# Performance work log

Measured on AMD Instinct MI355X. Metric: run time of the kernel, lower is better.

The kernel has to match this reference:

```python
import jax, jax.numpy as jnp
import numpy as np

N, C, H, W = 4, 256, 64, 64
C_EMBED = C // 2  # 128

def setup_inputs() -> dict:
    key = jax.random.key(0)
    k1, k2, k3, k4 = jax.random.split(key, 4)
    x = jax.random.normal(k1, (N, C, H, W), dtype=jnp.float32)
    # 1x1 conv weights stored as [out_ch, in_ch] (torch Conv2d weight squeezed)
    theta_w = jax.random.normal(k2, (C_EMBED, C), dtype=jnp.float32) * 0.01
    phi_w = jax.random.normal(k3, (C_EMBED, C), dtype=jnp.float32) * 0.01
    proj_w = jax.random.normal(k4, (C, C), dtype=jnp.float32) * 0.01
    return {"x": x, "theta_w": theta_w, "phi_w": phi_w, "proj_w": proj_w}

def reference(x, theta_w, phi_w, proj_w):
    n, c, h, w = x.shape
    s = h * w
    xf = x.reshape(n, c, s)  # [n, c, s]
    theta = jnp.einsum('ec,ncs->nse', theta_w, xf)  # [n, s, e]
    phi = jnp.einsum('ec,ncs->nes', phi_w, xf)      # [n, e, s]
    scale = jnp.sqrt(jnp.float32(theta_w.shape[0]))
    f = jnp.einsum('nse,net->nst', theta, phi) / scale  # [n, s, s]
    f = jax.nn.softmax(f, axis=-1)
    y = jnp.einsum('nst,nct->ncs', f, xf)  # attend over g = x, -> [n, c, s]
    res = jnp.einsum('oc,ncs->nos', proj_w, y)  # 1x1 projection conv
    return x + res.reshape(n, c, h, w)
```

## Files before the change

kernel.cpp:

```cpp
#include <hip/hip_runtime.h>
#include <cstdint>
#include <cstddef>

#define NB 4
#define CH 256
#define SS 4096
#define EE 128
#define QSCALE 0.08838834764831845f

typedef __attribute__((ext_vector_type(8))) short bfrag;
typedef __attribute__((ext_vector_type(8))) unsigned short u16x8;
typedef __attribute__((ext_vector_type(8))) _Float16 h16x8;
typedef __attribute__((ext_vector_type(4))) float f32x4;

__device__ __forceinline__ unsigned short f2bf(float f) {
  union { float f; unsigned int u; } v; v.f = f;
  unsigned int u = v.u;
  unsigned int r = u + 0x7FFFu + ((u >> 16) & 1u);
  return (unsigned short)(r >> 16);
}

__device__ __forceinline__ void lds_barrier() {
  asm volatile("s_waitcnt lgkmcnt(0)" ::: "memory");
  __builtin_amdgcn_s_barrier();
}

__global__ __launch_bounds__(256) void cvt_w(
    const float* __restrict__ thw, const float* __restrict__ phw,
    const float* __restrict__ pw,
    unsigned short* __restrict__ thwb, unsigned short* __restrict__ phwb,
    unsigned short* __restrict__ pwb)
{
  const int nw4 = EE * CH / 4;
  const int np4 = CH * CH / 4;
  int i = blockIdx.x * 256 + threadIdx.x;
  const float* src; unsigned short* dst; int off;
  if      (i < nw4)           { src = thw; dst = thwb; off = i; }
  else if (i < 2 * nw4)       { src = phw; dst = phwb; off = i - nw4; }
  else if (i < 2 * nw4 + np4) { src = pw;  dst = pwb;  off = i - 2 * nw4; }
  else return;
  float4 v = reinterpret_cast<const float4*>(src)[off];
  ushort4 o;
  o.x = f2bf(v.x); o.y = f2bf(v.y); o.z = f2bf(v.z); o.w = f2bf(v.w);
  reinterpret_cast<ushort4*>(dst)[off] = o;
}

__global__ __launch_bounds__(512) void pass1_qk(
    const float* __restrict__ x,
    const unsigned short* __restrict__ thw,
    const unsigned short* __restrict__ phw,
    unsigned short* __restrict__ xb,
    unsigned short* __restrict__ Qt,
    unsigned short* __restrict__ Kt)
{
  __shared__ unsigned short xT[64][CH + 8];
  const int t  = threadIdx.x;
  const int n  = blockIdx.y;
  const int s0 = blockIdx.x * 64;

  {
    const int soff = (t & 15) * 4;
    const int c0   = t >> 4;
    #pragma unroll
    for (int ci = 0; ci < 8; ++ci) {
      const int c = c0 + ci * 32;
      const size_t rowoff = ((size_t)n * CH + c) * SS + s0;
      float4 v = reinterpret_cast<const float4*>(x + rowoff)[soff >> 2];
      ushort4 o;
      o.x = f2bf(v.x); o.y = f2bf(v.y); o.z = f2bf(v.z); o.w = f2bf(v.w);
      reinterpret_cast<ushort4*>(xb + rowoff)[soff >> 2] = o;
      xT[soff + 0][c] = o.x;
      xT[soff + 1][c] = o.y;
      xT[soff + 2][c] = o.z;
      xT[soff + 3][c] = o.w;
    }
  }
  __syncthreads();

  const int w    = t >> 6;
  const int lane = t & 63;
  const int q    = lane >> 4;
  const int mr   = lane & 15;
  const int wrow = (w & 3) * 16;
  const int half = w >> 2;

  bfrag a[8];
  {
    const bfrag* rp = reinterpret_cast<const bfrag*>(&xT[wrow + mr][0]);
    #pragma unroll
    for (int k = 0; k < 8; ++k) a[k] = rp[k * 4 + q];
  }

  const unsigned short* wsel = half ? phw : thw;
  unsigned short*       osel = half ? Kt  : Qt;
  const float           sc   = half ? 1.0f : QSCALE;
  const bfrag* wp = reinterpret_cast<const bfrag*>(wsel);
  #pragma unroll
  for (int nt = 0; nt < 8; ++nt) {
    f32x4 acc = {0.f, 0.f, 0.f, 0.f};
    #pragma unroll
    for (int k = 0; k < 8; ++k) {
      bfrag b = wp[(nt * 16 + mr) * (CH / 8) + k * 4 + q];
      acc = __builtin_amdgcn_mfma_f32_16x16x32_bf16(a[k], b, acc, 0, 0, 0);
    }
    #pragma unroll
    for (int i = 0; i < 4; ++i) {
      const int srow = s0 + wrow + q * 4 + i;
      osel[((size_t)n * SS + srow) * EE + nt * 16 + mr] = f2bf(acc[i] * sc);
    }
  }
}

__global__ __launch_bounds__(512, 2) void pass2a(
    const unsigned short* __restrict__ Qt,
    const unsigned short* __restrict__ Kt,
    const unsigned short* __restrict__ xb,
    void* __restrict__ Opart_,
    float* __restrict__ ML,
    int use32)
{
  __shared__ __align__(16) unsigned char SMEM[138752];
  float          (*S_lds)[132] = reinterpret_cast<float(*)[132]>(SMEM);
  unsigned short (*P_lds)[136] = reinterpret_cast<unsigned short(*)[136]>(SMEM + 67584);
  unsigned short (*Q_lds)[136] = reinterpret_cast<unsigned short(*)[136]>(SMEM + 102400);
  float* row_m     = reinterpret_cast<float*>(SMEM + 137216);
  float* row_l     = reinterpret_cast<float*>(SMEM + 137728);
  float* row_alpha = reinterpret_cast<float*>(SMEM + 138240);

  float*    Of32 = reinterpret_cast<float*>(Opart_);
  _Float16* Oh16 = reinterpret_cast<_Float16*>(Opart_);

  const int t     = threadIdx.x;
  const int id    = blockIdx.x;
  const int xcd   = id & 7;
  const int n     = xcd >> 1;
  const int h     = xcd & 1;
  const int qt    = id >> 3;
  const int s0    = qt * 128;
  const int kbase = h * 2048;

  const int w    = t >> 6;
  const int lane = t & 63;
  const int q    = lane >> 4;
  const int mr   = lane & 15;

  if (t < 128) { row_m[t] = -INFINITY; row_l[t] = 0.f; }

  {
    const int col = (t & 15) * 8;
    #pragma unroll
    for (int j = 0; j < 4; ++j) {
      const int row = (t >> 4) + j * 32;
      *reinterpret_cast<u16x8*>(&Q_lds[row][col]) =
          *reinterpret_cast<const u16x8*>(
              Qt + ((size_t)n * SS + s0 + row) * EE + col);
    }
  }

  f32x4 o_accA[4][2], o_accB[4][2];
  #pragma unroll
  for (int ms = 0; ms < 4; ++ms)
    #pragma unroll
    for (int nt = 0; nt < 2; ++nt) {
      o_accA[ms][nt] = (f32x4){0.f, 0.f, 0.f, 0.f};
      o_accB[ms][nt] = (f32x4){0.f, 0.f, 0.f, 0.f};
    }

  __syncthreads();

  bfrag kb[4];
  {
    const bfrag* rp = reinterpret_cast<const bfrag*>(
        Kt + ((size_t)n * SS + kbase + w * 16 + mr) * EE);
    #pragma unroll
    for (int k = 0; k < 4; ++k) kb[k] = rp[k * 4 + q];
  }

#define QK_HALF(RB)                                                          \
  do {                                                                       \
    _Pragma("unroll")                                                        \
    for (int ms = 0; ms < 4; ++ms) {                                         \
      f32x4 acc = {0.f, 0.f, 0.f, 0.f};                                      \
      _Pragma("unroll")                                                      \
      for (int k = 0; k < 4; ++k) {                                          \
        bfrag aq = *reinterpret_cast<const bfrag*>(                          \
            &Q_lds[(RB) + ms * 16 + mr][(k * 4 + q) * 8]);                   \
        acc = __builtin_amdgcn_mfma_f32_16x16x32_bf16(aq, kb[k], acc, 0,0,0);\
      }                                                                      \
      _Pragma("unroll")                                                      \
      for (int i = 0; i < 4; ++i)                                            \
        S_lds[(RB) + ms * 16 + q * 4 + i][w * 16 + mr] = acc[i];             \
    }                                                                        \
  } while (0)

#define PV_HALF(OACC, RB)                                                    \
  do {                                                                       \
    _Pragma("unroll")                                                        \
    for (int ms = 0; ms < 4; ++ms) {                                         \
      float al[4];                                                           \
      _Pragma("unroll")                                                      \
      for (int i = 0; i < 4; ++i) al[i] = row_alpha[(RB) + ms*16 + q*4 + i]; \
      _Pragma("unroll")                                                      \
      for (int nt = 0; nt < 2; ++nt)                                         \
        _Pragma("unroll")                                                    \
        for (int i = 0; i < 4; ++i) OACC[ms][nt][i] *= al[i];                \
    }                                                                        \
    _Pragma("unroll")                                                        \
    for (int kk = 0; kk < 4; ++kk) {                                         \
      bfrag pa[4];                                                           \
      _Pragma("unroll")                                                      \
      for (int ms = 0; ms < 4; ++ms)                                         \
        pa[ms] = reinterpret_cast<const bfrag*>(                             \
            &P_lds[(RB) + ms * 16 + mr][0])[kk * 4 + q];                     \
      _Pragma("unroll")                                                      \
      for (int nt = 0; nt < 2; ++nt)                                         \
        _Pragma("unroll")                                                    \
        for (int ms = 0; ms < 4; ++ms)                                       \
          OACC[ms][nt] = __builtin_amdgcn_mfma_f32_16x16x32_bf16(            \
              pa[ms], vb[kk][nt], OACC[ms][nt], 0, 0, 0);                    \
    }                                                                        \
  } while (0)

  for (int t0 = 0; t0 < 2048; t0 += 128) {
    bfrag vb[4][2];
    #pragma unroll
    for (int nt = 0; nt < 2; ++nt) {
      const int c = w * 32 + nt * 16 + mr;
      const bfrag* vp = reinterpret_cast<const bfrag*>(
          xb + ((size_t)n * CH + c) * SS + kbase + t0);
      #pragma unroll
      for (int kk = 0; kk < 4; ++kk) vb[kk][nt] = vp[kk * 4 + q];
    }

    QK_HALF(0);
    QK_HALF(64);
    lds_barrier();

    if (t0 + 128 < 2048) {
      const bfrag* rp = reinterpret_cast<const bfrag*>(
          Kt + ((size_t)n * SS + kbase + t0 + 128 + w * 16 + mr) * EE);
      #pragma unroll
      for (int k = 0; k < 4; ++k) kb[k] = rp[k * 4 + q];
    }

    #pragma unroll
    for (int sh = 0; sh < 2; ++sh) {
      const int r  = sh * 64 + (t >> 3);
      const int cg = t & 7;
      const float4* srow = reinterpret_cast<const float4*>(&S_lds[r][cg * 16]);
      float4 v0 = srow[0], v1 = srow[1], v2 = srow[2], v3 = srow[3];
      float vmax = fmaxf(fmaxf(fmaxf(v0.x, v0.y), fmaxf(v0.z, v0.w)),
                         fmaxf(fmaxf(v1.x, v1.y), fmaxf(v1.z, v1.w)));
      vmax = fmaxf(vmax, fmaxf(fmaxf(fmaxf(v2.x, v2.y), fmaxf(v2.z, v2.w)),
                               fmaxf(fmaxf(v3.x, v3.y), fmaxf(v3.z, v3.w))));
      vmax = fmaxf(vmax, __shfl_xor(vmax, 1, 8));
      vmax = fmaxf(vmax, __shfl_xor(vmax, 2, 8));
      vmax = fmaxf(vmax, __shfl_xor(vmax, 4, 8));
      const float m_old = row_m[r];
      const float m_new = fmaxf(m_old, vmax);

      float p[16];
      p[0]=__expf(v0.x-m_new); p[1]=__expf(v0.y-m_new); p[2]=__expf(v0.z-m_new); p[3]=__expf(v0.w-m_new);
      p[4]=__expf(v1.x-m_new); p[5]=__expf(v1.y-m_new); p[6]=__expf(v1.z-m_new); p[7]=__expf(v1.w-m_new);
      p[8]=__expf(v2.x-m_new); p[9]=__expf(v2.y-m_new); p[10]=__expf(v2.z-m_new); p[11]=__expf(v2.w-m_new);
      p[12]=__expf(v3.x-m_new); p[13]=__expf(v3.y-m_new); p[14]=__expf(v3.z-m_new); p[15]=__expf(v3.w-m_new);
      float sum = 0.f;
      u16x8 pk0, pk1;
      #pragma unroll
      for (int j = 0; j < 8; ++j) { sum += p[j];     pk0[j] = f2bf(p[j]); }
      #pragma unroll
      for (int j = 0; j < 8; ++j) { sum += p[8 + j]; pk1[j] = f2bf(p[8 + j]); }
      *reinterpret_cast<u16x8*>(&P_lds[r][cg * 16])     = pk0;
      *reinterpret_cast<u16x8*>(&P_lds[r][cg * 16 + 8]) = pk1;
      sum += __shfl_xor(sum, 1, 8);
      sum += __shfl_xor(sum, 2, 8);
      sum += __shfl_xor(sum, 4, 8);
      if (cg == 0) {
        const float al = __expf(m_old - m_new);
        row_alpha[r] = al;
        row_m[r]     = m_new;
        row_l[r]     = row_l[r] * al + sum;
      }
    }
    lds_barrier();

    PV_HALF(o_accA, 0);
    PV_HALF(o_accB, 64);
  }

  const size_t p = ((size_t)(n * 32 + qt)) * 2 + h;

#define EPI_HALF(OACC, RB)                                                   \
  do {                                                                       \
    _Pragma("unroll")                                                        \
    for (int ms = 0; ms < 4; ++ms) {                                         \
      float inv[4];                                                          \
      _Pragma("unroll")                                                      \
      for (int i = 0; i < 4; ++i)                                            \
        inv[i] = 1.0f / row_l[(RB) + ms * 16 + q * 4 + i];                   \
      _Pragma("unroll")                                                      \
      for (int nt = 0; nt < 2; ++nt)                                         \
        _Pragma("unroll")                                                    \
        for (int i = 0; i < 4; ++i) {                                        \
          const size_t oi =                                                  \
              (p * 128 + (RB) + ms * 16 + q * 4 + i) * 256 +                 \
              w * 32 + nt * 16 + mr;                                         \
          const float yv = OACC[ms][nt][i] * inv[i];                         \
          if (use32) Of32[oi] = yv; else Oh16[oi] = (_Float16)yv;            \
        }                                                                    \
    }                                                                        \
  } while (0)

  EPI_HALF(o_accA, 0);
  EPI_HALF(o_accB, 64);
  if (t < 128) {
    ML[p * 256 + t * 2]     = row_m[t];
    ML[p * 256 + t * 2 + 1] = row_l[t];
  }
}

__global__ __launch_bounds__(512) void pass2b(
    const void* __restrict__ Opart_,
    const float* __restrict__ ML,
    const unsigned short* __restrict__ pwb,
    const float* __restrict__ x,
    float* __restrict__ out,
    int use32)
{
  __shared__ __align__(16) unsigned char SMEM[34816];
  unsigned short (*Y_lds)[CH + 8] =
      reinterpret_cast<unsigned short(*)[CH + 8]>(SMEM);
  float* w0 = reinterpret_cast<float*>(SMEM + 33792);
  float* w1 = reinterpret_cast<float*>(SMEM + 34048);

  const float*    Of32 = reinterpret_cast<const float*>(Opart_);
  const _Float16* Oh16 = reinterpret_cast<const _Float16*>(Opart_);

  const int t   = threadIdx.x;
  const int id  = blockIdx.x;
  const int n   = id >> 6;
  const int sub = id & 63;
  const int s0  = sub * 64;
  const int qt  = sub >> 1;
  const int rb  = (sub & 1) * 64;
  const size_t p0 = ((size_t)(n * 32 + qt)) * 2;

  if (t < 64) {
    const float ma = ML[p0 * 256 + (rb + t) * 2];
    const float la = ML[p0 * 256 + (rb + t) * 2 + 1];
    const float mb = ML[(p0 + 1) * 256 + (rb + t) * 2];
    const float lb = ML[(p0 + 1) * 256 + (rb + t) * 2 + 1];
    const float m  = fmaxf(ma, mb);
    const float e0 = __expf(ma - m) * la;
    const float e1 = __expf(mb - m) * lb;
    const float iL = 1.0f / (e0 + e1);
    w0[t] = e0 * iL;
    w1[t] = e1 * iL;
  }
  __syncthreads();

  {
    const int r = t >> 3;
    #pragma unroll
    for (int seg = 0; seg < 4; ++seg) {
      const int c0 = (t & 7) * 8 + seg * 64;
      const size_t ai = (p0 * 128 + rb + r) * 256 + c0;
      const size_t bi = ((p0 + 1) * 128 + rb + r) * 256 + c0;
      float fa[8], fb[8];
      if (use32) {
        #pragma unroll
        for (int j = 0; j < 8; ++j) { fa[j] = Of32[ai + j]; fb[j] = Of32[bi + j]; }
      } else {
        h16x8 ha = *reinterpret_cast<const h16x8*>(Oh16 + ai);
        h16x8 hb = *reinterpret_cast<const h16x8*>(Oh16 + bi);
        #pragma unroll
        for (int j = 0; j < 8; ++j) { fa[j] = (float)ha[j]; fb[j] = (float)hb[j]; }
      }
      u16x8 y;
      #pragma unroll
      for (int j = 0; j < 8; ++j) y[j] = f2bf(fa[j] * w0[r] + fb[j] * w1[r]);
      *reinterpret_cast<u16x8*>(&Y_lds[r][c0]) = y;
    }
  }
  __syncthreads();

  const int w    = t >> 6;
  const int lane = t & 63;
  const int q    = lane >> 4;
  const int mr   = lane & 15;
  #pragma unroll
  for (int ot = 0; ot < 2; ++ot) {
    const int o0 = w * 32 + ot * 16;
    bfrag a[8];
    {
      const bfrag* ap = reinterpret_cast<const bfrag*>(pwb + (o0 + mr) * CH);
      #pragma unroll
      for (int k = 0; k < 8; ++k) a[k] = ap[k * 4 + q];
    }
    #pragma unroll
    for (int st = 0; st < 4; ++st) {
      f32x4 acc = {0.f, 0.f, 0.f, 0.f};
      const bfrag* bp = reinterpret_cast<const bfrag*>(&Y_lds[st * 16 + mr][0]);
      #pragma unroll
      for (int k = 0; k < 8; ++k)
        acc = __builtin_amdgcn_mfma_f32_16x16x32_bf16(a[k], bp[k * 4 + q], acc, 0, 0, 0);
      #pragma unroll
      for (int i = 0; i < 4; ++i) {
        const int o = o0 + q * 4 + i;
        const int s = s0 + st * 16 + mr;
        const size_t idx = ((size_t)n * CH + o) * SS + s;
        out[idx] = x[idx] + acc[i];
      }
    }
  }
}

__global__ __launch_bounds__(512, 2) void pass2_full(
    const unsigned short* __restrict__ Qt,
    const unsigned short* __restrict__ Kt,
    const unsigned short* __restrict__ xb,
    const unsigned short* __restrict__ pwb,
    const float* __restrict__ x,
    float* __restrict__ out)
{
  __shared__ __align__(16) unsigned char SMEM[51968];
  float          (*S_lds)[132] = reinterpret_cast<float(*)[132]>(SMEM);
  unsigned short (*P_lds)[136] = reinterpret_cast<unsigned short(*)[136]>(SMEM + 33792);
  float* row_m     = reinterpret_cast<float*>(SMEM + 51200);
  float* row_l     = reinterpret_cast<float*>(SMEM + 51456);
  float* row_alpha = reinterpret_cast<float*>(SMEM + 51712);

  const int t    = threadIdx.x;
  const int id   = blockIdx.x;
  const int xcd  = id & 7;
  const int n    = xcd >> 1;
  const int s0   = ((id >> 3) * 2 + (xcd & 1)) * 64;
  const int w    = t >> 6;
  const int lane = t & 63;
  const int q    = lane >> 4;
  const int mr   = lane & 15;

  if (t < 64) { row_m[t] = -INFINITY; row_l[t] = 0.f; }

  bfrag qa[4][4];
  #pragma unroll
  for (int ms = 0; ms < 4; ++ms) {
    const bfrag* rp = reinterpret_cast<const bfrag*>(
        Qt + ((size_t)n * SS + s0 + ms * 16 + mr) * EE);
    #pragma unroll
    for (int k = 0; k < 4; ++k) qa[ms][k] = rp[k * 4 + q];
  }

  f32x4 o_acc[4][2];
  #pragma unroll
  for (int ms = 0; ms < 4; ++ms)
    #pragma unroll
    for (int nt = 0; nt < 2; ++nt) o_acc[ms][nt] = (f32x4){0.f, 0.f, 0.f, 0.f};

  bfrag kb[4];
  {
    const bfrag* rp = reinterpret_cast<const bfrag*>(
        Kt + ((size_t)n * SS + w * 16 + mr) * EE);
    #pragma unroll
    for (int k = 0; k < 4; ++k) kb[k] = rp[k * 4 + q];
  }

  for (int t0 = 0; t0 < SS; t0 += 128) {
    bfrag vb[4][2];
    #pragma unroll
    for (int nt = 0; nt < 2; ++nt) {
      const int c = w * 32 + nt * 16 + mr;
      const bfrag* vp = reinterpret_cast<const bfrag*>(
          xb + ((size_t)n * CH + c) * SS + t0);
      #pragma unroll
      for (int kk = 0; kk < 4; ++kk) vb[kk][nt] = vp[kk * 4 + q];
    }

    #pragma unroll
    for (int ms = 0; ms < 4; ++ms) {
      f32x4 acc = {0.f, 0.f, 0.f, 0.f};
      #pragma unroll
      for (int k = 0; k < 4; ++k)
        acc = __builtin_amdgcn_mfma_f32_16x16x32_bf16(qa[ms][k], kb[k], acc, 0, 0, 0);
      #pragma unroll
      for (int i = 0; i < 4; ++i)
        S_lds[ms * 16 + q * 4 + i][w * 16 + mr] = acc[i];
    }
    lds_barrier();

    {
      const int t1 = t0 + 128;
      if (t1 < SS) {
        const bfrag* rp = reinterpret_cast<const bfrag*>(
            Kt + ((size_t)n * SS + t1 + w * 16 + mr) * EE);
        #pragma unroll
        for (int k = 0; k < 4; ++k) kb[k] = rp[k * 4 + q];
      }
    }

    {
      const int r  = t >> 3;
      const int cg = t & 7;
      const float4* srow = reinterpret_cast<const float4*>(&S_lds[r][cg * 16]);
      float4 v0 = srow[0], v1 = srow[1], v2 = srow[2], v3 = srow[3];
      float vmax = fmaxf(fmaxf(fmaxf(v0.x, v0.y), fmaxf(v0.z, v0.w)),
                         fmaxf(fmaxf(v1.x, v1.y), fmaxf(v1.z, v1.w)));
      vmax = fmaxf(vmax, fmaxf(fmaxf(fmaxf(v2.x, v2.y), fmaxf(v2.z, v2.w)),
                               fmaxf(fmaxf(v3.x, v3.y), fmaxf(v3.z, v3.w))));
      vmax = fmaxf(vmax, __shfl_xor(vmax, 1, 8));
      vmax = fmaxf(vmax, __shfl_xor(vmax, 2, 8));
      vmax = fmaxf(vmax, __shfl_xor(vmax, 4, 8));
      const float m_old = row_m[r];
      const float m_new = fmaxf(m_old, vmax);

      float p[16];
      p[0]=__expf(v0.x-m_new); p[1]=__expf(v0.y-m_new); p[2]=__expf(v0.z-m_new); p[3]=__expf(v0.w-m_new);
      p[4]=__expf(v1.x-m_new); p[5]=__expf(v1.y-m_new); p[6]=__expf(v1.z-m_new); p[7]=__expf(v1.w-m_new);
      p[8]=__expf(v2.x-m_new); p[9]=__expf(v2.y-m_new); p[10]=__expf(v2.z-m_new); p[11]=__expf(v2.w-m_new);
      p[12]=__expf(v3.x-m_new); p[13]=__expf(v3.y-m_new); p[14]=__expf(v3.z-m_new); p[15]=__expf(v3.w-m_new);
      float sum = 0.f;
      u16x8 pk0, pk1;
      #pragma unroll
      for (int j = 0; j < 8; ++j) { sum += p[j];     pk0[j] = f2bf(p[j]); }
      #pragma unroll
      for (int j = 0; j < 8; ++j) { sum += p[8 + j]; pk1[j] = f2bf(p[8 + j]); }
      *reinterpret_cast<u16x8*>(&P_lds[r][cg * 16])     = pk0;
      *reinterpret_cast<u16x8*>(&P_lds[r][cg * 16 + 8]) = pk1;
      sum += __shfl_xor(sum, 1, 8);
      sum += __shfl_xor(sum, 2, 8);
      sum += __shfl_xor(sum, 4, 8);
      if (cg == 0) {
        const float al = __expf(m_old - m_new);
        row_alpha[r] = al;
        row_m[r]     = m_new;
        row_l[r]     = row_l[r] * al + sum;
      }
    }
    lds_barrier();

    #pragma unroll
    for (int ms = 0; ms < 4; ++ms) {
      float al[4];
      #pragma unroll
      for (int i = 0; i < 4; ++i) al[i] = row_alpha[ms * 16 + q * 4 + i];
      #pragma unroll
      for (int nt = 0; nt < 2; ++nt)
        #pragma unroll
        for (int i = 0; i < 4; ++i) o_acc[ms][nt][i] *= al[i];
    }

    #pragma unroll
    for (int kk = 0; kk < 4; ++kk) {
      bfrag pa[4];
      #pragma unroll
      for (int ms = 0; ms < 4; ++ms)
        pa[ms] = reinterpret_cast<const bfrag*>(&P_lds[ms * 16 + mr][0])[kk * 4 + q];
      #pragma unroll
      for (int nt = 0; nt < 2; ++nt)
        #pragma unroll
        for (int ms = 0; ms < 4; ++ms)
          o_acc[ms][nt] = __builtin_amdgcn_mfma_f32_16x16x32_bf16(
              pa[ms], vb[kk][nt], o_acc[ms][nt], 0, 0, 0);
    }
  }

  __syncthreads();
  unsigned short (*Y_lds)[CH + 8] =
      reinterpret_cast<unsigned short(*)[CH + 8]>(SMEM);

  #pragma unroll
  for (int ms = 0; ms < 4; ++ms) {
    float inv[4];
    #pragma unroll
    for (int i = 0; i < 4; ++i) inv[i] = 1.0f / row_l[ms * 16 + q * 4 + i];
    #pragma unroll
    for (int nt = 0; nt < 2; ++nt) {
      const int c = w * 32 + nt * 16 + mr;
      #pragma unroll
      for (int i = 0; i < 4; ++i)
        Y_lds[ms * 16 + q * 4 + i][c] = f2bf(o_acc[ms][nt][i] * inv[i]);
    }
  }
  __syncthreads();

  #pragma unroll
  for (int ot = 0; ot < 2; ++ot) {
    const int o0 = w * 32 + ot * 16;
    bfrag a[8];
    {
      const bfrag* ap = reinterpret_cast<const bfrag*>(pwb + (o0 + mr) * CH);
      #pragma unroll
      for (int k = 0; k < 8; ++k) a[k] = ap[k * 4 + q];
    }
    #pragma unroll
    for (int st = 0; st < 4; ++st) {
      f32x4 acc = {0.f, 0.f, 0.f, 0.f};
      const bfrag* bp = reinterpret_cast<const bfrag*>(&Y_lds[st * 16 + mr][0]);
      #pragma unroll
      for (int k = 0; k < 8; ++k)
        acc = __builtin_amdgcn_mfma_f32_16x16x32_bf16(a[k], bp[k * 4 + q], acc, 0, 0, 0);
      #pragma unroll
      for (int i = 0; i < 4; ++i) {
        const int o = o0 + q * 4 + i;
        const int s = s0 + st * 16 + mr;
        const size_t idx = ((size_t)n * CH + o) * SS + s;
        out[idx] = x[idx] + acc[i];
      }
    }
  }
}

extern "C" void kernel_launch(void* const* d_in, const int* in_sizes, int n_in,
                              void* d_out, int out_size, void* d_ws, size_t ws_size,
                              hipStream_t stream) {
  const float* x   = (const float*)d_in[0];
  const float* thw = (const float*)d_in[1];
  const float* phw = (const float*)d_in[2];
  const float* pw  = (const float*)d_in[3];
  float* out = (float*)d_out;

  unsigned short* xb   = (unsigned short*)d_ws;
  unsigned short* Qt   = xb + (size_t)NB * CH * SS;
  unsigned short* Kt   = Qt + (size_t)NB * SS * EE;
  unsigned short* thwb = Kt + (size_t)NB * SS * EE;
  unsigned short* phwb = thwb + EE * CH;
  unsigned short* pwb  = phwb + EE * CH;
  float*          ML   = (float*)(pwb + CH * CH);
  void*           Opart = (void*)(ML + (size_t)256 * 128 * 2);

  const size_t opart_off = (size_t)((char*)Opart - (char*)d_ws);
  const size_t opart_elems = (size_t)256 * 128 * 256;
  const int fits32 = ws_size >= opart_off + opart_elems * 4;
  const int fits16 = ws_size >= opart_off + opart_elems * 2;

  const int nw4 = EE * CH / 4;
  const int np4 = CH * CH / 4;
  const int totw4 = 2 * nw4 + np4;
  cvt_w<<<(totw4 + 255) / 256, 256, 0, stream>>>(thw, phw, pw, thwb, phwb, pwb);

  pass1_qk<<<dim3(SS / 64, NB), 512, 0, stream>>>(x, thwb, phwb, xb, Qt, Kt);

  if (fits32 || fits16) {
    const int use32 = fits32 ? 1 : 0;
    pass2a<<<dim3(256), 512, 0, stream>>>(Qt, Kt, xb, Opart, ML, use32);
    pass2b<<<dim3(256), 512, 0, stream>>>(Opart, ML, pwb, x, out, use32);
  } else {
    pass2_full<<<dim3(NB * SS / 64), 512, 0, stream>>>(Qt, Kt, xb, pwb, x, out);
  }
}
```

Before: 190.5 us.

## Keep Q fragments in registers and always store fp16 partial outputs

The QK^T stage now loads each wave's Q rows straight from global memory into registers, where they stay for the whole key loop. The Q tile is no longer staged in LDS, which shrinks shared memory by about 34KB and removes the per-iteration LDS reads of Q. Each wave now computes a 64x32 block of S instead of a 128x16 column strip. The partial-output buffer is forced to fp16, which halves its write and read traffic between pass2a and pass2b, even when the workspace could hold fp32. The cost is more register pressure, which could hurt occupancy under launch_bounds(512,2), plus the lower precision of always using fp16 partials.

Result: no change. 191.8 us (+0.7%).

```diff
diff --git a/kernel.cpp b/kernel.cpp
--- a/kernel.cpp
+++ b/kernel.cpp
@@ -115,20 +115,15 @@
     const unsigned short* __restrict__ Qt,
     const unsigned short* __restrict__ Kt,
     const unsigned short* __restrict__ xb,
-    void* __restrict__ Opart_,
-    float* __restrict__ ML,
-    int use32)
+    _Float16* __restrict__ Opart,
+    float* __restrict__ ML)
 {
-  __shared__ __align__(16) unsigned char SMEM[138752];
+  __shared__ __align__(16) unsigned char SMEM[103936];
   float          (*S_lds)[132] = reinterpret_cast<float(*)[132]>(SMEM);
   unsigned short (*P_lds)[136] = reinterpret_cast<unsigned short(*)[136]>(SMEM + 67584);
-  unsigned short (*Q_lds)[136] = reinterpret_cast<unsigned short(*)[136]>(SMEM + 102400);
-  float* row_m     = reinterpret_cast<float*>(SMEM + 137216);
-  float* row_l     = reinterpret_cast<float*>(SMEM + 137728);
-  float* row_alpha = reinterpret_cast<float*>(SMEM + 138240);
-
-  float*    Of32 = reinterpret_cast<float*>(Opart_);
-  _Float16* Oh16 = reinterpret_cast<_Float16*>(Opart_);
+  float* row_m     = reinterpret_cast<float*>(SMEM + 102400);
+  float* row_l     = reinterpret_cast<float*>(SMEM + 102912);
+  float* row_alpha = reinterpret_cast<float*>(SMEM + 103424);
 
   const int t     = threadIdx.x;
   const int id    = blockIdx.x;
@@ -139,22 +134,22 @@
   const int s0    = qt * 128;
   const int kbase = h * 2048;
 
-  const int w    = t >> 6;
-  const int lane = t & 63;
-  const int q    = lane >> 4;
-  const int mr   = lane & 15;
+  const int w      = t >> 6;
+  const int lane   = t & 63;
+  const int q      = lane >> 4;
+  const int mr     = lane & 15;
+  const int colblk = w & 3;
+  const int rb     = (w >> 2) * 64;
 
   if (t < 128) { row_m[t] = -INFINITY; row_l[t] = 0.f; }
 
-  {
-    const int col = (t & 15) * 8;
-    #pragma unroll
-    for (int j = 0; j < 4; ++j) {
-      const int row = (t >> 4) + j * 32;
-      *reinterpret_cast<u16x8*>(&Q_lds[row][col]) =
-          *reinterpret_cast<const u16x8*>(
-              Qt + ((size_t)n * SS + s0 + row) * EE + col);
-    }
+  bfrag qa[4][4];
+  #pragma unroll
+  for (int ms = 0; ms < 4; ++ms) {
+    const bfrag* rp = reinterpret_cast<const bfrag*>(
+        Qt + ((size_t)n * SS + s0 + rb + ms * 16 + mr) * EE);
+    #pragma unroll
+    for (int k = 0; k < 4; ++k) qa[ms][k] = rp[k * 4 + q];
   }
 
   f32x4 o_accA[4][2], o_accB[4][2];
@@ -168,30 +163,14 @@
 
   __syncthreads();
 
-  bfrag kb[4];
-  {
+  bfrag kb[4][2];
+  #pragma unroll
+  for (int nt = 0; nt < 2; ++nt) {
     const bfrag* rp = reinterpret_cast<const bfrag*>(
-        Kt + ((size_t)n * SS + kbase + w * 16 + mr) * EE);
-    #pragma unroll
-    for (int k = 0; k < 4; ++k) kb[k] = rp[k * 4 + q];
-  }
-
-#define QK_HALF(RB)                                                          \
-  do {                                                                       \
-    _Pragma("unroll")                                                        \
-    for (int ms = 0; ms < 4; ++ms) {                                         \
-      f32x4 acc = {0.f, 0.f, 0.f, 0.f};                                      \
-      _Pragma("unroll")                                                      \
-      for (int k = 0; k < 4; ++k) {                                          \
-        bfrag aq = *reinterpret_cast<const bfrag*>(                          \
-            &Q_lds[(RB) + ms * 16 + mr][(k * 4 + q) * 8]);                   \
-        acc = __builtin_amdgcn_mfma_f32_16x16x32_bf16(aq, kb[k], acc, 0,0,0);\
-      }                                                                      \
-      _Pragma("unroll")                                                      \
-      for (int i = 0; i < 4; ++i)                                            \
-        S_lds[(RB) + ms * 16 + q * 4 + i][w * 16 + mr] = acc[i];             \
-    }                                                                        \
-  } while (0)
+        Kt + ((size_t)n * SS + kbase + colblk * 32 + nt * 16 + mr) * EE);
+    #pragma unroll
+    for (int k = 0; k < 4; ++k) kb[k][nt] = rp[k * 4 + q];
+  }
 
 #define PV_HALF(OACC, RB)                                                    \
   do {                                                                       \
@@ -232,15 +211,31 @@
       for (int kk = 0; kk < 4; ++kk) vb[kk][nt] = vp[kk * 4 + q];
     }
 
-    QK_HALF(0);
-    QK_HALF(64);
+    #pragma unroll
+    for (int ms = 0; ms < 4; ++ms) {
+      f32x4 acc0 = {0.f, 0.f, 0.f, 0.f};
+      f32x4 acc1 = {0.f, 0.f, 0.f, 0.f};
+      #pragma unroll
+      for (int k = 0; k < 4; ++k) {
+        acc0 = __builtin_amdgcn_mfma_f32_16x16x32_bf16(qa[ms][k], kb[k][0], acc0, 0, 0, 0);
+        acc1 = __builtin_amdgcn_mfma_f32_16x16x32_bf16(qa[ms][k], kb[k][1], acc1, 0, 0, 0);
+      }
+      #pragma unroll
+      for (int i = 0; i < 4; ++i) {
+        S_lds[rb + ms * 16 + q * 4 + i][colblk * 32 + mr]      = acc0[i];
+        S_lds[rb + ms * 16 + q * 4 + i][colblk * 32 + 16 + mr] = acc1[i];
+      }
+    }
     lds_barrier();
 
     if (t0 + 128 < 2048) {
-      const bfrag* rp = reinterpret_cast<const bfrag*>(
-          Kt + ((size_t)n * SS + kbase + t0 + 128 + w * 16 + mr) * EE);
-      #pragma unroll
-      for (int k = 0; k < 4; ++k) kb[k] = rp[k * 4 + q];
+      #pragma unroll
+      for (int nt = 0; nt < 2; ++nt) {
+        const bfrag* rp = reinterpret_cast<const bfrag*>(
+            Kt + ((size_t)n * SS + kbase + t0 + 128 + colblk * 32 + nt * 16 + mr) * EE);
+        #pragma unroll
+        for (int k = 0; k < 4; ++k) kb[k][nt] = rp[k * 4 + q];
+      }
     }
 
     #pragma unroll
@@ -305,8 +300,7 @@
           const size_t oi =                                                  \
               (p * 128 + (RB) + ms * 16 + q * 4 + i) * 256 +                 \
               w * 32 + nt * 16 + mr;                                         \
-          const float yv = OACC[ms][nt][i] * inv[i];                         \
-          if (use32) Of32[oi] = yv; else Oh16[oi] = (_Float16)yv;            \
+          Opart[oi] = (_Float16)(OACC[ms][nt][i] * inv[i]);                  \
         }                                                                    \
     }                                                                        \
   } while (0)
@@ -320,21 +314,17 @@
 }
 
 __global__ __launch_bounds__(512) void pass2b(
-    const void* __restrict__ Opart_,
+    const _Float16* __restrict__ Opart,
     const float* __restrict__ ML,
     const unsigned short* __restrict__ pwb,
     const float* __restrict__ x,
-    float* __restrict__ out,
-    int use32)
+    float* __restrict__ out)
 {
   __shared__ __align__(16) unsigned char SMEM[34816];
   unsigned short (*Y_lds)[CH + 8] =
       reinterpret_cast<unsigned short(*)[CH + 8]>(SMEM);
   float* w0 = reinterpret_cast<float*>(SMEM + 33792);
   float* w1 = reinterpret_cast<float*>(SMEM + 34048);
-
-  const float*    Of32 = reinterpret_cast<const float*>(Opart_);
-  const _Float16* Oh16 = reinterpret_cast<const _Float16*>(Opart_);
 
   const int t   = threadIdx.x;
   const int id  = blockIdx.x;
@@ -366,19 +356,12 @@
       const int c0 = (t & 7) * 8 + seg * 64;
       const size_t ai = (p0 * 128 + rb + r) * 256 + c0;
       const size_t bi = ((p0 + 1) * 128 + rb + r) * 256 + c0;
-      float fa[8], fb[8];
-      if (use32) {
-        #pragma unroll
-        for (int j = 0; j < 8; ++j) { fa[j] = Of32[ai + j]; fb[j] = Of32[bi + j]; }
-      } else {
-        h16x8 ha = *reinterpret_cast<const h16x8*>(Oh16 + ai);
-        h16x8 hb = *reinterpret_cast<const h16x8*>(Oh16 + bi);
-        #pragma unroll
-        for (int j = 0; j < 8; ++j) { fa[j] = (float)ha[j]; fb[j] = (float)hb[j]; }
-      }
+      h16x8 ha = *reinterpret_cast<const h16x8*>(Opart + ai);
+      h16x8 hb = *reinterpret_cast<const h16x8*>(Opart + bi);
       u16x8 y;
       #pragma unroll
-      for (int j = 0; j < 8; ++j) y[j] = f2bf(fa[j] * w0[r] + fb[j] * w1[r]);
+      for (int j = 0; j < 8; ++j)
+        y[j] = f2bf((float)ha[j] * w0[r] + (float)hb[j] * w1[r]);
       *reinterpret_cast<u16x8*>(&Y_lds[r][c0]) = y;
     }
   }
@@ -626,12 +609,11 @@
   unsigned short* phwb = thwb + EE * CH;
   unsigned short* pwb  = phwb + EE * CH;
   float*          ML   = (float*)(pwb + CH * CH);
-  void*           Opart = (void*)(ML + (size_t)256 * 128 * 2);
+  _Float16*       Opart = (_Float16*)(ML + (size_t)256 * 128 * 2);
 
   const size_t opart_off = (size_t)((char*)Opart - (char*)d_ws);
-  const size_t opart_elems = (size_t)256 * 128 * 256;
-  const int fits32 = ws_size >= opart_off + opart_elems * 4;
-  const int fits16 = ws_size >= opart_off + opart_elems * 2;
+  const size_t opart_bytes = (size_t)256 * 128 * 256 * 2;
+  const int fits = ws_size >= opart_off + opart_bytes;
 
   const int nw4 = EE * CH / 4;
   const int np4 = CH * CH / 4;
@@ -640,10 +622,9 @@
 
   pass1_qk<<<dim3(SS / 64, NB), 512, 0, stream>>>(x, thwb, phwb, xb, Qt, Kt);
 
-  if (fits32 || fits16) {
-    const int use32 = fits32 ? 1 : 0;
-    pass2a<<<dim3(256), 512, 0, stream>>>(Qt, Kt, xb, Opart, ML, use32);
-    pass2b<<<dim3(256), 512, 0, stream>>>(Opart, ML, pwb, x, out, use32);
+  if (fits) {
+    pass2a<<<dim3(256), 512, 0, stream>>>(Qt, Kt, xb, Opart, ML);
+    pass2b<<<dim3(256), 512, 0, stream>>>(Opart, ML, pwb, x, out);
   } else {
     pass2_full<<<dim3(NB * SS / 64), 512, 0, stream>>>(Qt, Kt, xb, pwb, x, out);
   }
```

## Swizzle LDS tiles in pass2a and always store partial outputs in fp16

Applied to the files above, without the earlier changes.

Replaces the padded Q, S and P shared-memory arrays in pass2a with unpadded buffers addressed through an XOR swizzle on the row index, which avoids bank conflicts while using less LDS. It also drops the fp32 partial-output path, so the split attention partials are always written and read as fp16, halving that intermediate traffic when the workspace is large. The cost is lower precision in the partial accumulators and extra address arithmetic for the swizzle.

Result: faster. 180.1 us (-5.4%).

```diff
diff --git a/kernel.cpp b/kernel.cpp
--- a/kernel.cpp
+++ b/kernel.cpp
@@ -23,6 +23,11 @@
 __device__ __forceinline__ void lds_barrier() {
   asm volatile("s_waitcnt lgkmcnt(0)" ::: "memory");
   __builtin_amdgcn_s_barrier();
+}
+
+__device__ __forceinline__ unsigned char* swz(
+    unsigned char* base, int row, int rowStrideBytes, int byteInRow) {
+  return base + row * rowStrideBytes + (byteInRow ^ ((row & 7) << 4));
 }
 
 __global__ __launch_bounds__(256) void cvt_w(
@@ -115,20 +120,16 @@
     const unsigned short* __restrict__ Qt,
     const unsigned short* __restrict__ Kt,
     const unsigned short* __restrict__ xb,
-    void* __restrict__ Opart_,
-    float* __restrict__ ML,
-    int use32)
+    _Float16* __restrict__ Opart,
+    float* __restrict__ ML)
 {
-  __shared__ __align__(16) unsigned char SMEM[138752];
-  float          (*S_lds)[132] = reinterpret_cast<float(*)[132]>(SMEM);
-  unsigned short (*P_lds)[136] = reinterpret_cast<unsigned short(*)[136]>(SMEM + 67584);
-  unsigned short (*Q_lds)[136] = reinterpret_cast<unsigned short(*)[136]>(SMEM + 102400);
-  float* row_m     = reinterpret_cast<float*>(SMEM + 137216);
-  float* row_l     = reinterpret_cast<float*>(SMEM + 137728);
-  float* row_alpha = reinterpret_cast<float*>(SMEM + 138240);
-
-  float*    Of32 = reinterpret_cast<float*>(Opart_);
-  _Float16* Oh16 = reinterpret_cast<_Float16*>(Opart_);
+  __shared__ __align__(16) unsigned char SMEM[132608];
+  unsigned char* Qb = SMEM;
+  unsigned char* Sb = SMEM + 32768;
+  unsigned char* Pb = SMEM + 98304;
+  float* row_m     = reinterpret_cast<float*>(SMEM + 131072);
+  float* row_l     = reinterpret_cast<float*>(SMEM + 131584);
+  float* row_alpha = reinterpret_cast<float*>(SMEM + 132096);
 
   const int t     = threadIdx.x;
   const int id    = blockIdx.x;
@@ -147,13 +148,13 @@
   if (t < 128) { row_m[t] = -INFINITY; row_l[t] = 0.f; }
 
   {
-    const int col = (t & 15) * 8;
+    const int col = (t & 15) * 16;
     #pragma unroll
     for (int j = 0; j < 4; ++j) {
       const int row = (t >> 4) + j * 32;
-      *reinterpret_cast<u16x8*>(&Q_lds[row][col]) =
+      *reinterpret_cast<u16x8*>(swz(Qb, row, 256, col)) =
           *reinterpret_cast<const u16x8*>(
-              Qt + ((size_t)n * SS + s0 + row) * EE + col);
+              Qt + ((size_t)n * SS + s0 + row) * EE + (col >> 1));
     }
   }
 
@@ -184,12 +185,14 @@
       _Pragma("unroll")                                                      \
       for (int k = 0; k < 4; ++k) {                                          \
         bfrag aq = *reinterpret_cast<const bfrag*>(                          \
-            &Q_lds[(RB) + ms * 16 + mr][(k * 4 + q) * 8]);                   \
+            swz(Qb, (RB) + ms * 16 + mr, 256, (k * 4 + q) * 16));            \
         acc = __builtin_amdgcn_mfma_f32_16x16x32_bf16(aq, kb[k], acc, 0,0,0);\
       }                                                                      \
       _Pragma("unroll")                                                      \
       for (int i = 0; i < 4; ++i)                                            \
-        S_lds[(RB) + ms * 16 + q * 4 + i][w * 16 + mr] = acc[i];             \
+        *reinterpret_cast<float*>(                                           \
+            swz(Sb, (RB) + ms * 16 + q * 4 + i, 512, (w * 16 + mr) * 4)) =   \
+            acc[i];                                                          \
     }                                                                        \
   } while (0)
 
@@ -210,8 +213,8 @@
       bfrag pa[4];                                                           \
       _Pragma("unroll")                                                      \
       for (int ms = 0; ms < 4; ++ms)                                         \
-        pa[ms] = reinterpret_cast<const bfrag*>(                             \
-            &P_lds[(RB) + ms * 16 + mr][0])[kk * 4 + q];                     \
+        pa[ms] = *reinterpret_cast<const bfrag*>(                            \
+            swz(Pb, (RB) + ms * 16 + mr, 256, (kk * 4 + q) * 16));           \
       _Pragma("unroll")                                                      \
       for (int nt = 0; nt < 2; ++nt)                                         \
         _Pragma("unroll")                                                    \
@@ -247,8 +250,10 @@
     for (int sh = 0; sh < 2; ++sh) {
       const int r  = sh * 64 + (t >> 3);
       const int cg = t & 7;
-      const float4* srow = reinterpret_cast<const float4*>(&S_lds[r][cg * 16]);
-      float4 v0 = srow[0], v1 = srow[1], v2 = srow[2], v3 = srow[3];
+      float4 v0 = *reinterpret_cast<const float4*>(swz(Sb, r, 512, cg * 64));
+      float4 v1 = *reinterpret_cast<const float4*>(swz(Sb, r, 512, cg * 64 + 16));
+      float4 v2 = *reinterpret_cast<const float4*>(swz(Sb, r, 512, cg * 64 + 32));
+      float4 v3 = *reinterpret_cast<const float4*>(swz(Sb, r, 512, cg * 64 + 48));
       float vmax = fmaxf(fmaxf(fmaxf(v0.x, v0.y), fmaxf(v0.z, v0.w)),
                          fmaxf(fmaxf(v1.x, v1.y), fmaxf(v1.z, v1.w)));
       vmax = fmaxf(vmax, fmaxf(fmaxf(fmaxf(v2.x, v2.y), fmaxf(v2.z, v2.w)),
@@ -270,8 +275,8 @@
       for (int j = 0; j < 8; ++j) { sum += p[j];     pk0[j] = f2bf(p[j]); }
       #pragma unroll
       for (int j = 0; j < 8; ++j) { sum += p[8 + j]; pk1[j] = f2bf(p[8 + j]); }
-      *reinterpret_cast<u16x8*>(&P_lds[r][cg * 16])     = pk0;
-      *reinterpret_cast<u16x8*>(&P_lds[r][cg * 16 + 8]) = pk1;
+      *reinterpret_cast<u16x8*>(swz(Pb, r, 256, cg * 32))      = pk0;
+      *reinterpret_cast<u16x8*>(swz(Pb, r, 256, cg * 32 + 16)) = pk1;
       sum += __shfl_xor(sum, 1, 8);
       sum += __shfl_xor(sum, 2, 8);
       sum += __shfl_xor(sum, 4, 8);
@@ -305,8 +310,7 @@
           const size_t oi =                                                  \
               (p * 128 + (RB) + ms * 16 + q * 4 + i) * 256 +                 \
               w * 32 + nt * 16 + mr;                                         \
-          const float yv = OACC[ms][nt][i] * inv[i];                         \
-          if (use32) Of32[oi] = yv; else Oh16[oi] = (_Float16)yv;            \
+          Opart[oi] = (_Float16)(OACC[ms][nt][i] * inv[i]);                  \
         }                                                                    \
     }                                                                        \
   } while (0)
@@ -320,21 +324,17 @@
 }
 
 __global__ __launch_bounds__(512) void pass2b(
-    const void* __restrict__ Opart_,
+    const _Float16* __restrict__ Opart,
     const float* __restrict__ ML,
     const unsigned short* __restrict__ pwb,
     const float* __restrict__ x,
-    float* __restrict__ out,
-    int use32)
+    float* __restrict__ out)
 {
   __shared__ __align__(16) unsigned char SMEM[34816];
   unsigned short (*Y_lds)[CH + 8] =
       reinterpret_cast<unsigned short(*)[CH + 8]>(SMEM);
   float* w0 = reinterpret_cast<float*>(SMEM + 33792);
   float* w1 = reinterpret_cast<float*>(SMEM + 34048);
-
-  const float*    Of32 = reinterpret_cast<const float*>(Opart_);
-  const _Float16* Oh16 = reinterpret_cast<const _Float16*>(Opart_);
 
   const int t   = threadIdx.x;
   const int id  = blockIdx.x;
@@ -366,19 +366,12 @@
       const int c0 = (t & 7) * 8 + seg * 64;
       const size_t ai = (p0 * 128 + rb + r) * 256 + c0;
       const size_t bi = ((p0 + 1) * 128 + rb + r) * 256 + c0;
-      float fa[8], fb[8];
-      if (use32) {
-        #pragma unroll
-        for (int j = 0; j < 8; ++j) { fa[j] = Of32[ai + j]; fb[j] = Of32[bi + j]; }
-      } else {
-        h16x8 ha = *reinterpret_cast<const h16x8*>(Oh16 + ai);
-        h16x8 hb = *reinterpret_cast<const h16x8*>(Oh16 + bi);
-        #pragma unroll
-        for (int j = 0; j < 8; ++j) { fa[j] = (float)ha[j]; fb[j] = (float)hb[j]; }
-      }
+      h16x8 ha = *reinterpret_cast<const h16x8*>(Opart + ai);
+      h16x8 hb = *reinterpret_cast<const h16x8*>(Opart + bi);
       u16x8 y;
       #pragma unroll
-      for (int j = 0; j < 8; ++j) y[j] = f2bf(fa[j] * w0[r] + fb[j] * w1[r]);
+      for (int j = 0; j < 8; ++j)
+        y[j] = f2bf((float)ha[j] * w0[r] + (float)hb[j] * w1[r]);
       *reinterpret_cast<u16x8*>(&Y_lds[r][c0]) = y;
     }
   }
@@ -626,12 +619,11 @@
   unsigned short* phwb = thwb + EE * CH;
   unsigned short* pwb  = phwb + EE * CH;
   float*          ML   = (float*)(pwb + CH * CH);
-  void*           Opart = (void*)(ML + (size_t)256 * 128 * 2);
+  _Float16*       Opart = (_Float16*)(ML + (size_t)256 * 128 * 2);
 
   const size_t opart_off = (size_t)((char*)Opart - (char*)d_ws);
-  const size_t opart_elems = (size_t)256 * 128 * 256;
-  const int fits32 = ws_size >= opart_off + opart_elems * 4;
-  const int fits16 = ws_size >= opart_off + opart_elems * 2;
+  const size_t opart_bytes = (size_t)256 * 128 * 256 * 2;
+  const int fits = ws_size >= opart_off + opart_bytes;
 
   const int nw4 = EE * CH / 4;
   const int np4 = CH * CH / 4;
@@ -640,10 +632,9 @@
 
   pass1_qk<<<dim3(SS / 64, NB), 512, 0, stream>>>(x, thwb, phwb, xb, Qt, Kt);
 
-  if (fits32 || fits16) {
-    const int use32 = fits32 ? 1 : 0;
-    pass2a<<<dim3(256), 512, 0, stream>>>(Qt, Kt, xb, Opart, ML, use32);
-    pass2b<<<dim3(256), 512, 0, stream>>>(Opart, ML, pwb, x, out, use32);
+  if (fits) {
+    pass2a<<<dim3(256), 512, 0, stream>>>(Qt, Kt, xb, Opart, ML);
+    pass2b<<<dim3(256), 512, 0, stream>>>(Opart, ML, pwb, x, out);
   } else {
     pass2_full<<<dim3(NB * SS / 64), 512, 0, stream>>>(Qt, Kt, xb, pwb, x, out);
   }
```
